# Optimization experiments

Measured on AMD Instinct MI355X. Metric: run time of the kernel, lower is better.

## Reference

```python
import jax, jax.numpy as jnp
import numpy as np

B, S, D_MODEL = 2, 2048, 2048
N_HEADS, N_KV = 16, 4
HEAD_DIM = D_MODEL // N_HEADS  # 128
N_REP = N_HEADS // N_KV        # 4


def _apply_rope(x, cos, sin):
    # x: [B, H, S, Dh]; cos/sin: [S, Dh//2]
    c = cos[None, None, :, :]
    s = sin[None, None, :, :]
    x_even = x[..., ::2]
    x_odd = x[..., 1::2]
    re = x_even * c - x_odd * s
    ro = x_even * s + x_odd * c
    # interleave back: stack on last axis then flatten -> [..., Dh]
    return jnp.stack([re, ro], axis=-1).reshape(x.shape)


def setup_inputs() -> dict:
    key = jax.random.key(0)
    ks = jax.random.split(key, 7)
    std = 1.0 / np.sqrt(D_MODEL)
    return {
        "x": jax.random.normal(ks[0], (B, S, D_MODEL), dtype=jnp.float32),
        "rope_cos": jax.random.uniform(ks[1], (S, HEAD_DIM // 2), dtype=jnp.float32),
        "rope_sin": jax.random.uniform(ks[2], (S, HEAD_DIM // 2), dtype=jnp.float32),
        "Wq": jax.random.normal(ks[3], (D_MODEL, N_HEADS * HEAD_DIM), dtype=jnp.float32) * std,
        "Wk": jax.random.normal(ks[4], (D_MODEL, N_KV * HEAD_DIM), dtype=jnp.float32) * std,
        "Wv": jax.random.normal(ks[5], (D_MODEL, N_KV * HEAD_DIM), dtype=jnp.float32) * std,
        "Wo": jax.random.normal(ks[6], (N_HEADS * HEAD_DIM, D_MODEL), dtype=jnp.float32) * std,
    }


def reference(x, rope_cos, rope_sin, Wq, Wk, Wv, Wo):
    batch, seq_len, _ = x.shape
    q = (x @ Wq).reshape(batch, seq_len, N_HEADS, HEAD_DIM).transpose(0, 2, 1, 3)
    k = (x @ Wk).reshape(batch, seq_len, N_KV, HEAD_DIM).transpose(0, 2, 1, 3)
    v = (x @ Wv).reshape(batch, seq_len, N_KV, HEAD_DIM).transpose(0, 2, 1, 3)

    q = _apply_rope(q, rope_cos[:seq_len], rope_sin[:seq_len])
    k = _apply_rope(k, rope_cos[:seq_len], rope_sin[:seq_len])

    # GQA: group q heads by kv head instead of materializing repeated k/v.
    qg = q.reshape(batch, N_KV, N_REP, seq_len, HEAD_DIM)
    scale = 1.0 / np.sqrt(HEAD_DIM)
    scores = jnp.einsum('bgrqd,bgkd->bgrqk', qg, k) * scale

    causal = jnp.tril(jnp.ones((seq_len, seq_len), dtype=bool))
    scores = jnp.where(causal[None, None, None, :, :], scores, -jnp.inf)
    weights = jax.nn.softmax(scores, axis=-1)

    out = jnp.einsum('bgrqk,bgkd->bgrqd', weights, v)
    out = out.reshape(batch, N_HEADS, seq_len, HEAD_DIM).transpose(0, 2, 1, 3)
    out = out.reshape(batch, seq_len, N_HEADS * HEAD_DIM)
    return out @ Wo
```

## Files before the change

### kernel.cpp

```cpp
#include <hip/hip_runtime.h>
#include <hip/hip_bf16.h>
#include <math.h>

typedef __bf16 bf16x8_t __attribute__((ext_vector_type(8)));
typedef float f32x4 __attribute__((ext_vector_type(4)));
typedef unsigned short ushort8 __attribute__((ext_vector_type(8)));

__device__ inline unsigned short f2bf(float f) {
  unsigned int u = __builtin_bit_cast(unsigned int, f);
  u += 0x7fffu + ((u >> 16) & 1u);
  return (unsigned short)(u >> 16);
}
__device__ inline float b2f(unsigned short s) {
  unsigned int u = ((unsigned int)s) << 16;
  return __builtin_bit_cast(float, u);
}
__device__ inline unsigned int pack2bf(float lo, float hi) {
  return (unsigned int)f2bf(lo) | ((unsigned int)f2bf(hi) << 16);
}

__device__ __forceinline__ void gll16(const void* g, void* l) {
  __builtin_amdgcn_global_load_lds((const __attribute__((address_space(1))) void*)g,
                                   (__attribute__((address_space(3))) void*)l, 16, 0, 0);
}

__global__ __launch_bounds__(256) void prep_k(const float* __restrict__ x,
                                              const float* __restrict__ Wq,
                                              const float* __restrict__ Wk,
                                              const float* __restrict__ Wv,
                                              const float* __restrict__ Wo,
                                              unsigned short* __restrict__ xb,
                                              unsigned short* __restrict__ WallT,
                                              unsigned short* __restrict__ WoT) {
  const int bid = blockIdx.x;
  const int tid = threadIdx.x;
  if (bid < 10240) {
    __shared__ float tile[32][33];
    const int K = 2048;
    int y = bid / 64;
    int k0 = (bid % 64) * 32;
    const float* W;
    unsigned short* dst;
    int srcN, col0, dstRow0;
    if (y < 64) { W = Wq; srcN = 2048; col0 = y * 32; dst = WallT; dstRow0 = y * 32; }
    else if (y < 80) { W = Wk; srcN = 512; col0 = (y - 64) * 32; dst = WallT; dstRow0 = 2048 + (y - 64) * 32; }
    else if (y < 96) { W = Wv; srcN = 512; col0 = (y - 80) * 32; dst = WallT; dstRow0 = 2560 + (y - 80) * 32; }
    else { W = Wo; srcN = 2048; col0 = (y - 96) * 32; dst = WoT; dstRow0 = (y - 96) * 32; }
    int tx = tid & 31, ty = tid >> 5;
#pragma unroll
    for (int i = 0; i < 32; i += 8) tile[ty + i][tx] = W[(size_t)(k0 + ty + i) * srcN + col0 + tx];
    __syncthreads();
#pragma unroll
    for (int i = 0; i < 32; i += 8)
      dst[(size_t)(dstRow0 + ty + i) * K + k0 + tx] = f2bf(tile[tx][ty + i]);
  } else {
    int i = (bid - 10240) * 256 + tid;
    const float4* p = (const float4*)x + 2 * (size_t)i;
    float4 a = p[0], b = p[1];
    ushort8 v;
    v[0] = f2bf(a.x); v[1] = f2bf(a.y); v[2] = f2bf(a.z); v[3] = f2bf(a.w);
    v[4] = f2bf(b.x); v[5] = f2bf(b.y); v[6] = f2bf(b.z); v[7] = f2bf(b.w);
    ((ushort8*)xb)[i] = v;
  }
}

template <bool OUT_BF16, bool ROPE>
__global__ __launch_bounds__(256) void gemm_tn(const unsigned short* __restrict__ A,
                                               const unsigned short* __restrict__ Bt,
                                               void* __restrict__ Cv, int M, int N, int K,
                                               const float* __restrict__ cs,
                                               const float* __restrict__ sn, int ropeLim) {
  __shared__ __align__(16) unsigned short As[2][128 * 32];
  __shared__ __align__(16) unsigned short Bs[2][128 * 32];
  const int t = threadIdx.x, w = t >> 6, lane = t & 63;
  const int la = lane & 15, lk = lane >> 4;
  const int wr = w >> 1, wc = w & 1;
  const int nwg = gridDim.x * gridDim.y;
  const int flat = blockIdx.y * gridDim.x + blockIdx.x;
  const int swz = (flat & 7) * (nwg >> 3) + (flat >> 3);
  const int bxs = swz % gridDim.x, bys = swz / gridDim.x;
  const int bm = bys * 128, bn = bxs * 128;
  const int lrow = lane >> 2, lcb = (lane & 3) * 8;

  const unsigned short* Ab = A + (size_t)(bm + (w * 2) * 16 + lrow) * K + lcb;
  const unsigned short* Ab1 = A + (size_t)(bm + (w * 2 + 1) * 16 + lrow) * K + lcb;
  const unsigned short* Bb = Bt + (size_t)(bn + (w * 2) * 16 + lrow) * K + lcb;
  const unsigned short* Bb1 = Bt + (size_t)(bn + (w * 2 + 1) * 16 + lrow) * K + lcb;
  const int c0 = w * 2, c1 = w * 2 + 1;

  f32x4 acc[4][4] = {};

  gll16(Ab, (char*)As[0] + c0 * 1024);
  gll16(Ab1, (char*)As[0] + c1 * 1024);
  gll16(Bb, (char*)Bs[0] + c0 * 1024);
  gll16(Bb1, (char*)Bs[0] + c1 * 1024);

  const int nt = K / 32;
  int cur = 0;
  for (int kt = 0; kt < nt; ++kt) {
    __syncthreads();
    if (kt + 1 < nt) {
      const int kn = (kt + 1) * 32;
      gll16(Ab + kn, (char*)As[cur ^ 1] + c0 * 1024);
      gll16(Ab1 + kn, (char*)As[cur ^ 1] + c1 * 1024);
      gll16(Bb + kn, (char*)Bs[cur ^ 1] + c0 * 1024);
      gll16(Bb1 + kn, (char*)Bs[cur ^ 1] + c1 * 1024);
    }

    bf16x8_t a[4], b[4];
#pragma unroll
    for (int m = 0; m < 4; ++m)
      a[m] = __builtin_bit_cast(
          bf16x8_t, *(const ushort8*)(As[cur] + (wr * 64 + m * 16 + la) * 32 + lk * 8));
#pragma unroll
    for (int n = 0; n < 4; ++n)
      b[n] = __builtin_bit_cast(
          bf16x8_t, *(const ushort8*)(Bs[cur] + (wc * 64 + n * 16 + la) * 32 + lk * 8));
#pragma unroll
    for (int m = 0; m < 4; ++m)
#pragma unroll
      for (int n = 0; n < 4; ++n)
        acc[m][n] = __builtin_amdgcn_mfma_f32_16x16x32_bf16(a[m], b[n], acc[m][n], 0, 0, 0);
    cur ^= 1;
  }

#pragma unroll
  for (int m = 0; m < 4; ++m) {
#pragma unroll
    for (int n = 0; n < 4; ++n) {
      const int col = bn + wc * 64 + n * 16 + la;
      const bool doRope = ROPE && (col < ropeLim);
#pragma unroll
      for (int r = 0; r < 4; ++r) {
        int row = bm + wr * 64 + m * 16 + lk * 4 + r;
        float val = acc[m][n][r];
        if (ROPE) {
          float pval = __shfl_xor(val, 1);
          if (doRope) {
            int srow = row & 2047;
            int i = (col & 127) >> 1;
            float cc = cs[srow * 64 + i], ss = sn[srow * 64 + i];
            val = (la & 1) ? (pval * ss + val * cc) : (val * cc - pval * ss);
          }
        }
        if (OUT_BF16)
          ((unsigned short*)Cv)[(size_t)row * N + col] = f2bf(val);
        else
          ((float*)Cv)[(size_t)row * N + col] = val;
      }
    }
  }
}

__global__ void transpose_v(const unsigned short* __restrict__ QKV, unsigned short* __restrict__ Vt) {
  __shared__ unsigned short tile[32][33];
  int bg = blockIdx.z;
  int b = bg >> 2, g = bg & 3;
  int s0 = blockIdx.x * 32, d0 = blockIdx.y * 32;
  int tx = threadIdx.x, ty = threadIdx.y;
#pragma unroll
  for (int i = 0; i < 32; i += 8)
    tile[ty + i][tx] = QKV[((size_t)(b * 2048 + s0 + ty + i)) * 3072 + 2560 + g * 128 + d0 + tx];
  __syncthreads();
#pragma unroll
  for (int i = 0; i < 32; i += 8)
    Vt[((size_t)(bg * 128 + d0 + ty + i)) * 2048 + s0 + tx] = tile[tx][ty + i];
}

__global__ __launch_bounds__(256, 2) void attn_mfma(const unsigned short* __restrict__ QKV,
                                                    const unsigned short* __restrict__ Vt,
                                                    unsigned short* __restrict__ Ob) {
  const int S = 2048;
  __shared__ __align__(16) unsigned short Ks[2][64 * 128];
  __shared__ __align__(16) unsigned short Vs[2][128 * 64];
  __shared__ __align__(16) unsigned short Ps[4 * 32 * 64];

  const int t = threadIdx.x;
  const int w = t >> 6, lane = t & 63;
  const int la = lane & 15, lk = lane >> 4;
  const int b = blockIdx.z, h = blockIdx.y, g = h >> 2;
  const int qt = (b == 0) ? (gridDim.x - 1 - blockIdx.x) : blockIdx.x;
  const int q0 = qt * 128;
  const int qw = q0 + w * 32;
  const float scale = 0.08838834764831845f;

  const unsigned short* ksrc[4];
  const unsigned short* vsrc[4];
#pragma unroll
  for (int u = 0; u < 4; ++u) {
    int kr = 16 * w + 4 * u + (lane >> 4);
    int kp = lane & 15;
    ksrc[u] = QKV + (size_t)(b * S + kr) * 3072 + 2048 + g * 128 + (kp ^ (kr & 7)) * 8;
    int vr = 32 * w + 8 * u + (lane >> 3);
    int vp = lane & 7;
    vsrc[u] = Vt + (size_t)((b * 4 + g) * 128 + vr) * 2048 + (vp ^ (vr & 7)) * 8;
  }

  bf16x8_t qf[2][4];
#pragma unroll
  for (int qi = 0; qi < 2; ++qi)
#pragma unroll
    for (int dt = 0; dt < 4; ++dt)
      qf[qi][dt] = __builtin_bit_cast(
          bf16x8_t, *(const ushort8*)(QKV + (size_t)(b * S + qw + qi * 16 + la) * 3072 + h * 128 +
                                      dt * 32 + lk * 8));

  f32x4 oa[2][8];
#pragma unroll
  for (int qi = 0; qi < 2; ++qi)
#pragma unroll
    for (int dt = 0; dt < 8; ++dt) oa[qi][dt] = (f32x4){0.f, 0.f, 0.f, 0.f};
  float mr[2] = {-1e30f, -1e30f}, lr[2] = {0.f, 0.f};

  const int n_kt = 2 * qt + 2;
  const int kmask0 = qw & ~63;
  char* pw = (char*)Ps + w * 4096;

#pragma unroll
  for (int u = 0; u < 4; ++u) {
    gll16(ksrc[u], (char*)Ks[0] + (4 * w + u) * 1024);
    gll16(vsrc[u], (char*)Vs[0] + (4 * w + u) * 1024);
  }
  __syncthreads();

  int cur = 0;
  for (int kt = 0; kt < n_kt; ++kt) {
    const int k0 = kt * 64;
    if (kt + 1 < n_kt) {
      const int kn = k0 + 64;
#pragma unroll
      for (int u = 0; u < 4; ++u) {
        gll16(ksrc[u] + (size_t)kn * 3072, (char*)Ks[cur ^ 1] + (4 * w + u) * 1024);
        gll16(vsrc[u] + kn, (char*)Vs[cur ^ 1] + (4 * w + u) * 1024);
      }
    }

    if (k0 <= qw + 31) {
      char* Ksb = (char*)Ks[cur];
      char* Vsb = (char*)Vs[cur];

      f32x4 sacc[2][4];
#pragma unroll
      for (int qi = 0; qi < 2; ++qi)
#pragma unroll
        for (int ktc = 0; ktc < 4; ++ktc) sacc[qi][ktc] = (f32x4){0.f, 0.f, 0.f, 0.f};
      __builtin_amdgcn_s_setprio(1);
#pragma unroll
      for (int ktc = 0; ktc < 4; ++ktc) {
        int row = ktc * 16 + la;
#pragma unroll
        for (int dt = 0; dt < 4; ++dt) {
          bf16x8_t kf = __builtin_bit_cast(
              bf16x8_t, *(const ushort8*)(Ksb + row * 256 + ((((dt << 2) + lk) ^ (row & 7)) << 4)));
          sacc[0][ktc] = __builtin_amdgcn_mfma_f32_16x16x32_bf16(kf, qf[0][dt], sacc[0][ktc], 0, 0, 0);
          sacc[1][ktc] = __builtin_amdgcn_mfma_f32_16x16x32_bf16(kf, qf[1][dt], sacc[1][ktc], 0, 0, 0);
        }
      }
      __builtin_amdgcn_s_setprio(0);

      const bool domask = (k0 == kmask0);
#pragma unroll
      for (int qi = 0; qi < 2; ++qi) {
        const int q = qw + qi * 16 + la;
        float p[4][4];
        float tm = -1e30f;
#pragma unroll
        for (int ktc = 0; ktc < 4; ++ktc)
#pragma unroll
          for (int r = 0; r < 4; ++r) {
            float sv = sacc[qi][ktc][r] * scale;
            if (domask && (k0 + ktc * 16 + lk * 4 + r > q)) sv = -1e30f;
            p[ktc][r] = sv;
            tm = fmaxf(tm, sv);
          }
        tm = fmaxf(tm, __shfl_xor(tm, 16));
        tm = fmaxf(tm, __shfl_xor(tm, 32));
        float mn;
        if (__all(tm - mr[qi] <= 8.f)) {
          mn = mr[qi];
        } else {
          mn = fmaxf(mr[qi], tm);
          float sc = __expf(mr[qi] - mn);
          mr[qi] = mn;
          lr[qi] *= sc;
          float scb[4];
#pragma unroll
          for (int r = 0; r < 4; ++r) scb[r] = __shfl(sc, lk * 4 + r);
#pragma unroll
          for (int dt = 0; dt < 8; ++dt)
#pragma unroll
            for (int r = 0; r < 4; ++r) oa[qi][dt][r] *= scb[r];
        }
        float ts = 0.f;
#pragma unroll
        for (int ktc = 0; ktc < 4; ++ktc)
#pragma unroll
          for (int r = 0; r < 4; ++r) {
            float e = __expf(p[ktc][r] - mn);
            p[ktc][r] = e;
            ts += e;
          }
        ts += __shfl_xor(ts, 16);
        ts += __shfl_xor(ts, 32);
        lr[qi] += ts;
        char* pq = pw + (qi * 16 + la) * 128;
#pragma unroll
        for (int ktc = 0; ktc < 4; ++ktc) {
          uint2 gv;
          gv.x = pack2bf(p[ktc][0], p[ktc][1]);
          gv.y = pack2bf(p[ktc][2], p[ktc][3]);
          *(uint2*)(pq + ((32 * ktc + 8 * lk) ^ ((la & 7) << 4))) = gv;
        }
      }
      asm volatile("s_waitcnt lgkmcnt(0)" ::: "memory");

      bf16x8_t pf[2][2];
#pragma unroll
      for (int qi = 0; qi < 2; ++qi)
#pragma unroll
        for (int ks = 0; ks < 2; ++ks)
          pf[qi][ks] = __builtin_bit_cast(
              bf16x8_t, *(const ushort8*)(pw + (qi * 16 + la) * 128 +
                                          ((64 * ks + 16 * lk) ^ ((la & 7) << 4))));
      __builtin_amdgcn_s_setprio(1);
#pragma unroll
      for (int dt = 0; dt < 8; ++dt) {
        int d = dt * 16 + la;
#pragma unroll
        for (int ks = 0; ks < 2; ++ks) {
          bf16x8_t vf = __builtin_bit_cast(
              bf16x8_t, *(const ushort8*)(Vsb + d * 128 + ((((ks << 2) + lk) ^ (d & 7)) << 4)));
          oa[0][dt] = __builtin_amdgcn_mfma_f32_16x16x32_bf16(pf[0][ks], vf, oa[0][dt], 0, 0, 0);
          oa[1][dt] = __builtin_amdgcn_mfma_f32_16x16x32_bf16(pf[1][ks], vf, oa[1][dt], 0, 0, 0);
        }
      }
      __builtin_amdgcn_s_setprio(0);
    }

    __syncthreads();
    cur ^= 1;
  }

#pragma unroll
  for (int qi = 0; qi < 2; ++qi) {
    float inv = 1.f / lr[qi];
    float invb[4];
#pragma unroll
    for (int r = 0; r < 4; ++r) invb[r] = __shfl(inv, lk * 4 + r);
#pragma unroll
    for (int dt = 0; dt < 8; ++dt)
#pragma unroll
      for (int r = 0; r < 4; ++r)
        Ob[(size_t)(b * S + qw + qi * 16 + lk * 4 + r) * 2048 + h * 128 + dt * 16 + la] =
            f2bf(oa[qi][dt][r] * invb[r]);
  }
}

extern "C" void kernel_launch(void* const* d_in, const int* in_sizes, int n_in,
                              void* d_out, int out_size, void* d_ws, size_t ws_size,
                              hipStream_t stream) {
  const float* x = (const float*)d_in[0];
  const float* rc = (const float*)d_in[1];
  const float* rs = (const float*)d_in[2];
  const float* Wq = (const float*)d_in[3];
  const float* Wk = (const float*)d_in[4];
  const float* Wv = (const float*)d_in[5];
  const float* Wo = (const float*)d_in[6];
  float* out = (float*)d_out;

  const int B = 2, S = 2048, DM = 2048;
  const int M = B * S;

  unsigned short* xb = (unsigned short*)d_ws;
  unsigned short* QKV = xb + (size_t)M * DM;
  unsigned short* WallT = QKV + (size_t)M * 3072;
  unsigned short* WoT = WallT + (size_t)3072 * DM;
  unsigned short* Vt = WallT + (size_t)2048 * 2048;
  unsigned short* Ob = xb;

  dim3 blk(256);

  prep_k<<<dim3(14336), blk, 0, stream>>>(x, Wq, Wk, Wv, Wo, xb, WallT, WoT);

  gemm_tn<true, true><<<dim3(3072 / 128, M / 128), blk, 0, stream>>>(xb, WallT, QKV, M, 3072, DM,
                                                                     rc, rs, 2560);

  transpose_v<<<dim3(S / 32, 4, B * 4), dim3(32, 8), 0, stream>>>(QKV, Vt);

  attn_mfma<<<dim3(S / 128, 16, B), dim3(256), 0, stream>>>(QKV, Vt, Ob);

  gemm_tn<false, false><<<dim3(DM / 128, M / 128), blk, 0, stream>>>(Ob, WoT, out, M, DM, DM,
                                                                     nullptr, nullptr, 0);
}
```

Before: 225.8 us.

## Shrink attention tiles to 64 queries and 32 keys, raise occupancy

The attention kernel now works on 64-query blocks with 16 queries per wave and 32-key tiles, down from 128 queries and 64-key tiles. LDS use and register pressure drop so launch bounds can ask for 4 blocks per CU, and the grid doubles to 32 query tiles per head. Query-tile order is also reshuffled across head and batch groups to balance the causal workload. In exchange each K/V tile is reused by fewer queries, which adds K/V traffic and per-tile sync and softmax overhead.

```diff
diff --git a/kernel.cpp b/kernel.cpp
--- a/kernel.cpp
+++ b/kernel.cpp
@@ -167,172 +167,157 @@
     Vt[((size_t)(bg * 128 + d0 + ty + i)) * 2048 + s0 + tx] = tile[tx][ty + i];
 }
 
-__global__ __launch_bounds__(256, 2) void attn_mfma(const unsigned short* __restrict__ QKV,
+__global__ __launch_bounds__(256, 4) void attn_mfma(const unsigned short* __restrict__ QKV,
                                                     const unsigned short* __restrict__ Vt,
                                                     unsigned short* __restrict__ Ob) {
   const int S = 2048;
-  __shared__ __align__(16) unsigned short Ks[2][64 * 128];
-  __shared__ __align__(16) unsigned short Vs[2][128 * 64];
-  __shared__ __align__(16) unsigned short Ps[4 * 32 * 64];
+  __shared__ __align__(16) unsigned short Ks[2][32 * 128];
+  __shared__ __align__(16) unsigned short Vs[2][128 * 32];
+  __shared__ __align__(16) unsigned short Ps[4 * 16 * 32];
 
   const int t = threadIdx.x;
   const int w = t >> 6, lane = t & 63;
   const int la = lane & 15, lk = lane >> 4;
   const int b = blockIdx.z, h = blockIdx.y, g = h >> 2;
-  const int qt = (b == 0) ? (gridDim.x - 1 - blockIdx.x) : blockIdx.x;
-  const int q0 = qt * 128;
-  const int qw = q0 + w * 32;
+  const int x = blockIdx.x;
+  const int hb = ((h >> 3) & 1) | ((b & 1) << 1);
+  int qt;
+  if (hb == 0) qt = x;
+  else if (hb == 1) qt = 31 - x;
+  else if (hb == 2) qt = (x + 16) & 31;
+  else qt = 31 - ((x + 16) & 31);
+  const int qw = qt * 64 + w * 16;
   const float scale = 0.08838834764831845f;
 
-  const unsigned short* ksrc[4];
-  const unsigned short* vsrc[4];
-#pragma unroll
-  for (int u = 0; u < 4; ++u) {
-    int kr = 16 * w + 4 * u + (lane >> 4);
+  const unsigned short* ksrc[2];
+  const unsigned short* vsrc[2];
+#pragma unroll
+  for (int u = 0; u < 2; ++u) {
+    int kr = (2 * w + u) * 4 + (lane >> 4);
     int kp = lane & 15;
     ksrc[u] = QKV + (size_t)(b * S + kr) * 3072 + 2048 + g * 128 + (kp ^ (kr & 7)) * 8;
-    int vr = 32 * w + 8 * u + (lane >> 3);
-    int vp = lane & 7;
-    vsrc[u] = Vt + (size_t)((b * 4 + g) * 128 + vr) * 2048 + (vp ^ (vr & 7)) * 8;
-  }
-
-  bf16x8_t qf[2][4];
-#pragma unroll
-  for (int qi = 0; qi < 2; ++qi)
-#pragma unroll
-    for (int dt = 0; dt < 4; ++dt)
-      qf[qi][dt] = __builtin_bit_cast(
-          bf16x8_t, *(const ushort8*)(QKV + (size_t)(b * S + qw + qi * 16 + la) * 3072 + h * 128 +
-                                      dt * 32 + lk * 8));
-
-  f32x4 oa[2][8];
-#pragma unroll
-  for (int qi = 0; qi < 2; ++qi)
-#pragma unroll
-    for (int dt = 0; dt < 8; ++dt) oa[qi][dt] = (f32x4){0.f, 0.f, 0.f, 0.f};
-  float mr[2] = {-1e30f, -1e30f}, lr[2] = {0.f, 0.f};
+    int vr = (2 * w + u) * 16 + (lane >> 2);
+    int vp = lane & 3;
+    vsrc[u] = Vt + (size_t)((b * 4 + g) * 128 + vr) * 2048 + (vp ^ (vr & 3)) * 8;
+  }
+
+  bf16x8_t qf[4];
+#pragma unroll
+  for (int dt = 0; dt < 4; ++dt)
+    qf[dt] = __builtin_bit_cast(
+        bf16x8_t,
+        *(const ushort8*)(QKV + (size_t)(b * S + qw + la) * 3072 + h * 128 + dt * 32 + lk * 8));
+
+  f32x4 oa[8];
+#pragma unroll
+  for (int dt = 0; dt < 8; ++dt) oa[dt] = (f32x4){0.f, 0.f, 0.f, 0.f};
+  float mr = -1e30f, lr = 0.f;
 
   const int n_kt = 2 * qt + 2;
-  const int kmask0 = qw & ~63;
-  char* pw = (char*)Ps + w * 4096;
-
-#pragma unroll
-  for (int u = 0; u < 4; ++u) {
-    gll16(ksrc[u], (char*)Ks[0] + (4 * w + u) * 1024);
-    gll16(vsrc[u], (char*)Vs[0] + (4 * w + u) * 1024);
+  const int kmask0 = qw & ~31;
+  char* pw = (char*)Ps + w * 1024;
+
+#pragma unroll
+  for (int u = 0; u < 2; ++u) {
+    gll16(ksrc[u], (char*)Ks[0] + (2 * w + u) * 1024);
+    gll16(vsrc[u], (char*)Vs[0] + (2 * w + u) * 1024);
   }
   __syncthreads();
 
   int cur = 0;
   for (int kt = 0; kt < n_kt; ++kt) {
-    const int k0 = kt * 64;
+    const int k0 = kt * 32;
     if (kt + 1 < n_kt) {
-      const int kn = k0 + 64;
-#pragma unroll
-      for (int u = 0; u < 4; ++u) {
-        gll16(ksrc[u] + (size_t)kn * 3072, (char*)Ks[cur ^ 1] + (4 * w + u) * 1024);
-        gll16(vsrc[u] + kn, (char*)Vs[cur ^ 1] + (4 * w + u) * 1024);
+      const int kn = k0 + 32;
+#pragma unroll
+      for (int u = 0; u < 2; ++u) {
+        gll16(ksrc[u] + (size_t)kn * 3072, (char*)Ks[cur ^ 1] + (2 * w + u) * 1024);
+        gll16(vsrc[u] + kn, (char*)Vs[cur ^ 1] + (2 * w + u) * 1024);
       }
     }
 
-    if (k0 <= qw + 31) {
+    if (k0 <= qw + 15) {
       char* Ksb = (char*)Ks[cur];
       char* Vsb = (char*)Vs[cur];
 
-      f32x4 sacc[2][4];
-#pragma unroll
-      for (int qi = 0; qi < 2; ++qi)
-#pragma unroll
-        for (int ktc = 0; ktc < 4; ++ktc) sacc[qi][ktc] = (f32x4){0.f, 0.f, 0.f, 0.f};
+      f32x4 sacc[2];
+#pragma unroll
+      for (int ktc = 0; ktc < 2; ++ktc) sacc[ktc] = (f32x4){0.f, 0.f, 0.f, 0.f};
       __builtin_amdgcn_s_setprio(1);
 #pragma unroll
-      for (int ktc = 0; ktc < 4; ++ktc) {
+      for (int ktc = 0; ktc < 2; ++ktc) {
         int row = ktc * 16 + la;
 #pragma unroll
         for (int dt = 0; dt < 4; ++dt) {
           bf16x8_t kf = __builtin_bit_cast(
               bf16x8_t, *(const ushort8*)(Ksb + row * 256 + ((((dt << 2) + lk) ^ (row & 7)) << 4)));
-          sacc[0][ktc] = __builtin_amdgcn_mfma_f32_16x16x32_bf16(kf, qf[0][dt], sacc[0][ktc], 0, 0, 0);
-          sacc[1][ktc] = __builtin_amdgcn_mfma_f32_16x16x32_bf16(kf, qf[1][dt], sacc[1][ktc], 0, 0, 0);
+          sacc[ktc] = __builtin_amdgcn_mfma_f32_16x16x32_bf16(kf, qf[dt], sacc[ktc], 0, 0, 0);
         }
       }
       __builtin_amdgcn_s_setprio(0);
 
       const bool domask = (k0 == kmask0);
-#pragma unroll
-      for (int qi = 0; qi < 2; ++qi) {
-        const int q = qw + qi * 16 + la;
-        float p[4][4];
-        float tm = -1e30f;
-#pragma unroll
-        for (int ktc = 0; ktc < 4; ++ktc)
-#pragma unroll
-          for (int r = 0; r < 4; ++r) {
-            float sv = sacc[qi][ktc][r] * scale;
-            if (domask && (k0 + ktc * 16 + lk * 4 + r > q)) sv = -1e30f;
-            p[ktc][r] = sv;
-            tm = fmaxf(tm, sv);
-          }
-        tm = fmaxf(tm, __shfl_xor(tm, 16));
-        tm = fmaxf(tm, __shfl_xor(tm, 32));
-        float mn;
-        if (__all(tm - mr[qi] <= 8.f)) {
-          mn = mr[qi];
-        } else {
-          mn = fmaxf(mr[qi], tm);
-          float sc = __expf(mr[qi] - mn);
-          mr[qi] = mn;
-          lr[qi] *= sc;
-          float scb[4];
-#pragma unroll
-          for (int r = 0; r < 4; ++r) scb[r] = __shfl(sc, lk * 4 + r);
-#pragma unroll
-          for (int dt = 0; dt < 8; ++dt)
-#pragma unroll
-            for (int r = 0; r < 4; ++r) oa[qi][dt][r] *= scb[r];
+      const int q = qw + la;
+      float p[2][4];
+      float tm = -1e30f;
+#pragma unroll
+      for (int ktc = 0; ktc < 2; ++ktc)
+#pragma unroll
+        for (int r = 0; r < 4; ++r) {
+          float sv = sacc[ktc][r] * scale;
+          if (domask && (k0 + ktc * 16 + lk * 4 + r > q)) sv = -1e30f;
+          p[ktc][r] = sv;
+          tm = fmaxf(tm, sv);
         }
-        float ts = 0.f;
-#pragma unroll
-        for (int ktc = 0; ktc < 4; ++ktc)
-#pragma unroll
-          for (int r = 0; r < 4; ++r) {
-            float e = __expf(p[ktc][r] - mn);
-            p[ktc][r] = e;
-            ts += e;
-          }
-        ts += __shfl_xor(ts, 16);
-        ts += __shfl_xor(ts, 32);
-        lr[qi] += ts;
-        char* pq = pw + (qi * 16 + la) * 128;
-#pragma unroll
-        for (int ktc = 0; ktc < 4; ++ktc) {
-          uint2 gv;
-          gv.x = pack2bf(p[ktc][0], p[ktc][1]);
-          gv.y = pack2bf(p[ktc][2], p[ktc][3]);
-          *(uint2*)(pq + ((32 * ktc + 8 * lk) ^ ((la & 7) << 4))) = gv;
+      tm = fmaxf(tm, __shfl_xor(tm, 16));
+      tm = fmaxf(tm, __shfl_xor(tm, 32));
+      float mn;
+      if (__all(tm - mr <= 8.f)) {
+        mn = mr;
+      } else {
+        mn = fmaxf(mr, tm);
+        float sc = __expf(mr - mn);
+        mr = mn;
+        lr *= sc;
+        float scb[4];
+#pragma unroll
+        for (int r = 0; r < 4; ++r) scb[r] = __shfl(sc, lk * 4 + r);
+#pragma unroll
+        for (int dt = 0; dt < 8; ++dt)
+#pragma unroll
+          for (int r = 0; r < 4; ++r) oa[dt][r] *= scb[r];
+      }
+      float ts = 0.f;
+#pragma unroll
+      for (int ktc = 0; ktc < 2; ++ktc)
+#pragma unroll
+        for (int r = 0; r < 4; ++r) {
+          float e = __expf(p[ktc][r] - mn);
+          p[ktc][r] = e;
+          ts += e;
         }
+      ts += __shfl_xor(ts, 16);
+      ts += __shfl_xor(ts, 32);
+      lr += ts;
+      char* pq = pw + la * 64;
+#pragma unroll
+      for (int ktc = 0; ktc < 2; ++ktc) {
+        uint2 gv;
+        gv.x = pack2bf(p[ktc][0], p[ktc][1]);
+        gv.y = pack2bf(p[ktc][2], p[ktc][3]);
+        *(uint2*)(pq + (((ktc * 2 + (lk >> 1)) ^ (la & 3)) << 4) + ((lk & 1) << 3)) = gv;
       }
       asm volatile("s_waitcnt lgkmcnt(0)" ::: "memory");
 
-      bf16x8_t pf[2][2];
-#pragma unroll
-      for (int qi = 0; qi < 2; ++qi)
-#pragma unroll
-        for (int ks = 0; ks < 2; ++ks)
-          pf[qi][ks] = __builtin_bit_cast(
-              bf16x8_t, *(const ushort8*)(pw + (qi * 16 + la) * 128 +
-                                          ((64 * ks + 16 * lk) ^ ((la & 7) << 4))));
+      bf16x8_t pf = __builtin_bit_cast(
+          bf16x8_t, *(const ushort8*)(pw + la * 64 + ((lk ^ (la & 3)) << 4)));
       __builtin_amdgcn_s_setprio(1);
 #pragma unroll
       for (int dt = 0; dt < 8; ++dt) {
         int d = dt * 16 + la;
-#pragma unroll
-        for (int ks = 0; ks < 2; ++ks) {
-          bf16x8_t vf = __builtin_bit_cast(
-              bf16x8_t, *(const ushort8*)(Vsb + d * 128 + ((((ks << 2) + lk) ^ (d & 7)) << 4)));
-          oa[0][dt] = __builtin_amdgcn_mfma_f32_16x16x32_bf16(pf[0][ks], vf, oa[0][dt], 0, 0, 0);
-          oa[1][dt] = __builtin_amdgcn_mfma_f32_16x16x32_bf16(pf[1][ks], vf, oa[1][dt], 0, 0, 0);
-        }
+        bf16x8_t vf = __builtin_bit_cast(
+            bf16x8_t, *(const ushort8*)(Vsb + d * 64 + ((lk ^ (d & 3)) << 4)));
+        oa[dt] = __builtin_amdgcn_mfma_f32_16x16x32_bf16(pf, vf, oa[dt], 0, 0, 0);
       }
       __builtin_amdgcn_s_setprio(0);
     }
@@ -341,19 +326,16 @@
     cur ^= 1;
   }
 
-#pragma unroll
-  for (int qi = 0; qi < 2; ++qi) {
-    float inv = 1.f / lr[qi];
-    float invb[4];
-#pragma unroll
-    for (int r = 0; r < 4; ++r) invb[r] = __shfl(inv, lk * 4 + r);
-#pragma unroll
-    for (int dt = 0; dt < 8; ++dt)
-#pragma unroll
-      for (int r = 0; r < 4; ++r)
-        Ob[(size_t)(b * S + qw + qi * 16 + lk * 4 + r) * 2048 + h * 128 + dt * 16 + la] =
-            f2bf(oa[qi][dt][r] * invb[r]);
-  }
+  float inv = 1.f / lr;
+  float invb[4];
+#pragma unroll
+  for (int r = 0; r < 4; ++r) invb[r] = __shfl(inv, lk * 4 + r);
+#pragma unroll
+  for (int dt = 0; dt < 8; ++dt)
+#pragma unroll
+    for (int r = 0; r < 4; ++r)
+      Ob[(size_t)(b * S + qw + lk * 4 + r) * 2048 + h * 128 + dt * 16 + la] =
+          f2bf(oa[dt][r] * invb[r]);
 }
 
 extern "C" void kernel_launch(void* const* d_in, const int* in_sizes, int n_in,
@@ -387,7 +369,7 @@
 
   transpose_v<<<dim3(S / 32, 4, B * 4), dim3(32, 8), 0, stream>>>(QKV, Vt);
 
-  attn_mfma<<<dim3(S / 128, 16, B), dim3(256), 0, stream>>>(QKV, Vt, Ob);
+  attn_mfma<<<dim3(32, 16, B), dim3(256), 0, stream>>>(QKV, Vt, Ob);
 
   gemm_tn<false, false><<<dim3(DM / 128, M / 128), blk, 0, stream>>>(Ob, WoT, out, M, DM, DM,
                                                                      nullptr, nullptr, 0);
```

New measurement: 239.1 us. +5.9%, slower.
